# Kernel optimization log

Hardware: AMD Instinct MI355X
Metric: run time of the kernel (lower is better)

The kernel has to match this reference:

```python
import jax, jax.numpy as jnp
import numpy as np

N, E, F, H, RBF = 50000, 400000, 128, 8, 100
HD = F // H
CUTOFF = 6.0

def _xavier(k, shape):
    fan_out, fan_in = shape
    lim = (6.0 / (fan_in + fan_out)) ** 0.5
    return jax.random.uniform(k, shape, minval=-lim, maxval=lim, dtype=jnp.float32)

def setup_inputs():
    key = jax.random.key(0)
    ks = jax.random.split(key, 16)
    x = jax.random.normal(ks[0], (N, F), jnp.float32)
    vec = jax.random.normal(ks[1], (N, 3, F), jnp.float32)
    edge_index = jax.random.randint(ks[2], (2, E), 0, N, dtype=jnp.int32)
    r_ij = jax.random.uniform(ks[3], (E,), jnp.float32) * CUTOFF
    d_ij = jax.random.normal(ks[4], (E, 3), jnp.float32)
    d_ij = d_ij / jnp.linalg.norm(d_ij, axis=-1, keepdims=True)
    f_ij = jax.random.normal(ks[5], (E, RBF), jnp.float32)
    return dict(
        x=x, vec=vec, edge_index=edge_index, r_ij=r_ij, f_ij=f_ij, d_ij=d_ij,
        ln_w=jnp.ones((F,), jnp.float32), ln_b=jnp.zeros((F,), jnp.float32),
        Wq=_xavier(ks[6], (F, F)), bq=jnp.zeros((F,), jnp.float32),
        Wk=_xavier(ks[7], (F, F)), bk=jnp.zeros((F,), jnp.float32),
        Wv=_xavier(ks[8], (3 * F, F)), bv=jnp.zeros((3 * F,), jnp.float32),
        Wvec=_xavier(ks[9], (3 * F, F)), bvec=jnp.zeros((3 * F,), jnp.float32),
        Wo=_xavier(ks[10], (3 * F, F)), bo=jnp.zeros((3 * F,), jnp.float32),
        Wdk=_xavier(ks[11], (F, RBF)), bdk=jnp.zeros((F,), jnp.float32),
        Wdv=_xavier(ks[12], (3 * F, RBF)), bdv=jnp.zeros((3 * F,), jnp.float32),
    )

def _cutoff(r):
    # CosineCutoff with cutoff_lower=0
    return 0.5 * (jnp.cos(r * (jnp.pi / CUTOFF)) + 1.0) * (r < CUTOFF).astype(r.dtype)

def reference(x, vec, edge_index, r_ij, f_ij, d_ij, ln_w, ln_b, Wq, bq, Wk, bk,
              Wv, bv, Wvec, bvec, Wo, bo, Wdk, bdk, Wdv, bdv):
    src, dst = edge_index[0], edge_index[1]  # PyG: x_j = x[src], x_i = x[dst], aggregate at dst
    mu = x.mean(-1, keepdims=True)
    var = ((x - mu) ** 2).mean(-1, keepdims=True)
    xn = (x - mu) / jnp.sqrt(var + 1e-5) * ln_w + ln_b
    q = (xn @ Wq.T + bq).reshape(N, H, HD)
    k = (xn @ Wk.T + bk).reshape(N, H, HD)
    v = (xn @ Wv.T + bv).reshape(N, H, 3 * HD)
    vp = vec @ Wvec.T + bvec  # (N,3,3F)
    vec1, vec2, vec3 = vp[..., :F], vp[..., F:2 * F], vp[..., 2 * F:]
    vec_dot = (vec1 * vec2).sum(axis=1)  # (N,F)
    vec_h = vec.reshape(N, 3, H, HD)
    dk = jax.nn.silu(f_ij @ Wdk.T + bdk).reshape(E, H, HD)
    dv = jax.nn.silu(f_ij @ Wdv.T + bdv).reshape(E, H, 3 * HD)
    # edge-wise messages
    attn = jax.nn.silu((q[dst] * k[src] * dk).sum(-1)) * _cutoff(r_ij)[:, None]  # (E,H)
    v_j = v[src] * dv
    xm, v1m, v2m = v_j[..., :HD], v_j[..., HD:2 * HD], v_j[..., 2 * HD:]
    xm = xm * attn[..., None]  # (E,H,HD)
    vecm = vec_h[src] * v1m[:, None] + v2m[:, None] * d_ij[:, :, None, None]  # (E,3,H,HD)
    # scatter-add to destination nodes
    x_agg = jax.ops.segment_sum(xm.reshape(E, F), dst, num_segments=N)
    vec_agg = jax.ops.segment_sum(vecm.reshape(E, 3 * F), dst, num_segments=N).reshape(N, 3, F)
    o = x_agg @ Wo.T + bo
    o1, o2, o3 = o[:, :F], o[:, F:2 * F], o[:, 2 * F:]
    dx = vec_dot * o2 + o3
    dvec = vec3 * o1[:, None, :] + vec_agg
    return dx, dvec
```

## Files before the change

### kernel.cpp

```cpp
#include <hip/hip_runtime.h>

#define N_NODES 50000
#define N_EDGES 400000

typedef __bf16 bf16x8 __attribute__((ext_vector_type(8)));
typedef float f32x4 __attribute__((ext_vector_type(4)));

__device__ __forceinline__ float bflo(uint u){ union{uint i; float f;} v; v.i = u<<16; return v.f; }
__device__ __forceinline__ float bfhi(uint u){ union{uint i; float f;} v; v.i = u & 0xffff0000u; return v.f; }
__device__ __forceinline__ float bf2f(ushort u){ union{uint i; float f;} v; v.i = ((uint)u)<<16; return v.f; }
__device__ __forceinline__ ushort f2bf(float f){
  union{float f; uint i;} v; v.f = f;
  uint r = (v.i + 0x7fffu + ((v.i>>16)&1u))>>16;
  return (ushort)r;
}
__device__ __forceinline__ uint pack2(float a, float b){
  return (uint)f2bf(a) | ((uint)f2bf(b)<<16);
}

__global__ __launch_bounds__(256) void f32_to_bf16(
    const float* __restrict__ in, ushort* __restrict__ out, int n)
{
  int i = blockIdx.x*256 + threadIdx.x;
  if (i < n) out[i] = f2bf(in[i]);
}

__global__ __launch_bounds__(256) void convert_pad(
    const float* __restrict__ in, ushort* __restrict__ out,
    int rows, int Kin, int Kout)
{
  int i = blockIdx.x*256 + threadIdx.x;
  if (i >= rows*Kout) return;
  int r = i / Kout, c = i - r*Kout;
  out[i] = (c < Kin) ? f2bf(in[(size_t)r*Kin + c]) : (ushort)0;
}

__global__ __launch_bounds__(256) void ln_kernel(
    const float* __restrict__ x, const float* __restrict__ w,
    const float* __restrict__ b, ushort* __restrict__ xn)
{
  int n = blockIdx.x*4 + (threadIdx.x>>6);
  if (n >= N_NODES) return;
  int lane = threadIdx.x & 63;
  float2 xp = ((const float2*)x)[(size_t)n*64 + lane];
  float x0 = xp.x, x1 = xp.y;
  float s = x0 + x1, s2 = x0*x0 + x1*x1;
  #pragma unroll
  for (int off=1; off<64; off<<=1){ s += __shfl_xor(s,off); s2 += __shfl_xor(s2,off); }
  float mu  = s*(1.0f/128.0f);
  float var = s2*(1.0f/128.0f) - mu*mu;
  float inv = 1.0f/sqrtf(var + 1e-5f);
  float2 wp = ((const float2*)w)[lane];
  float2 bp = ((const float2*)b)[lane];
  float y0 = (x0-mu)*inv*wp.x + bp.x;
  float y1 = (x1-mu)*inv*wp.y + bp.y;
  ((uint*)xn)[(size_t)n*64 + lane] = pack2(y0, y1);
}

__global__ __launch_bounds__(256) void hist_kernel(
    const int* __restrict__ ei, int* __restrict__ cnt)
{
  int e = blockIdx.x*256 + threadIdx.x;
  if (e < N_EDGES) atomicAdd(&cnt[ei[N_EDGES + e]], 1);
}

__global__ __launch_bounds__(1024) void scan_kernel(
    const int* __restrict__ cnt, int* __restrict__ offs, int* __restrict__ cursor)
{
  __shared__ int wsum[16];
  __shared__ int carry_s;
  int tid = threadIdx.x, lane = tid & 63, wid = tid >> 6;
  if (tid == 0) carry_s = 0;
  __syncthreads();
  for (int base = 0; base < N_NODES; base += 1024){
    int i = base + tid;
    int v = (i < N_NODES) ? cnt[i] : 0;
    int x = v;
    #pragma unroll
    for (int o=1;o<64;o<<=1){ int t=__shfl_up(x,o); if (lane>=o) x+=t; }
    if (lane == 63) wsum[wid] = x;
    __syncthreads();
    if (wid == 0){
      int ws = (lane < 16) ? wsum[lane] : 0;
      #pragma unroll
      for (int o=1;o<16;o<<=1){ int t=__shfl_up(ws,o); if (lane>=o) ws+=t; }
      if (lane < 16) wsum[lane] = ws;
    }
    __syncthreads();
    int wpre = (wid > 0) ? wsum[wid-1] : 0;
    int exc = x + wpre - v;
    int total = wsum[15];
    int o_ = carry_s + exc;
    if (i < N_NODES){ offs[i] = o_; cursor[i] = o_; }
    __syncthreads();
    if (tid == 0) carry_s += total;
    __syncthreads();
  }
  if (tid == 0) offs[N_NODES] = carry_s;
}

__global__ __launch_bounds__(256) void scatter_kernel(
    const int* __restrict__ ei, const float* __restrict__ rij,
    const float* __restrict__ dij, int* __restrict__ cursor,
    int* __restrict__ perm, int* __restrict__ srcs, int* __restrict__ dsts,
    float4* __restrict__ ed)
{
  int e = blockIdx.x*256 + threadIdx.x;
  if (e >= N_EDGES) return;
  int d = ei[N_EDGES + e];
  int pos = atomicAdd(&cursor[d], 1);
  perm[pos] = e;
  srcs[pos] = ei[e];
  dsts[pos] = d;
  ed[pos] = make_float4(rij[e], dij[3*(size_t)e], dij[3*(size_t)e+1], dij[3*(size_t)e+2]);
}

__global__ __launch_bounds__(256) void gather_fij(
    int st, int len, const int* __restrict__ perm,
    const float* __restrict__ fij, ushort* __restrict__ out)
{
  int p = blockIdx.x*4 + (threadIdx.x>>6);
  if (p >= len) return;
  int lane = threadIdx.x & 63;
  int eo = perm[st + p];
  uint val = 0;
  if (lane < 50){
    float2 f = *(const float2*)(fij + (size_t)eo*100 + 2*lane);
    val = pack2(f.x, f.y);
  }
  ((uint*)out)[(size_t)p*64 + lane] = val;
}

#define LDP 40

template<int MODE, int AF32, int SWZ>
__global__ __launch_bounds__(256) void gemm_bt(
    const void* __restrict__ Av, const ushort* __restrict__ W,
    const ushort* __restrict__ W2,
    const float* __restrict__ bias, const float* __restrict__ bias2,
    void* Cptr, const void* aux1, void* aux2,
    int M, int K, int Nc)
{
  __shared__ ushort As[128*LDP];
  __shared__ ushort Bs[128*LDP];
  __shared__ ushort Bs2[(MODE==7) ? 128*LDP : 2];
  const int tid = threadIdx.x;
  int bx, by;
  if (SWZ){
    int nby = Nc >> 7;
    int nwg = gridDim.x;
    int id  = blockIdx.x;
    int q = nwg >> 3, r = nwg & 7;
    int xcd = id & 7, iq = id >> 3;
    int base = (xcd < r) ? xcd*(q+1) : r*(q+1) + (xcd - r)*q;
    int L = base + iq;
    bx = L / nby; by = L - bx*nby;
  } else { bx = blockIdx.x; by = blockIdx.y; }
  const int row0 = bx*128, col0 = by*128;
  const int wave = tid>>6, lane = tid&63;
  const int wm = (wave>>1)*64, wn = (wave&1)*64;
  const int lr = lane&15, lq = lane>>4;
  f32x4 acc[4][4] = {};
  f32x4 acc2[4][4] = {};

  for (int k0=0; k0<K; k0+=32){
    #pragma unroll
    for (int rnd=0; rnd<2; rnd++){
      int e4 = (rnd*256 + tid)*8;
      int r = e4>>5, c = e4&31;
      int gk = k0 + c;
      {
        int gr = row0 + r;
        if (AF32){
          const float* Af = (const float*)Av;
          uint2 lo, hi;
          if (gr < M && gk + 8 <= K){
            const float* p = Af + (size_t)gr*K + gk;
            float4 f0 = *(const float4*)p;
            float4 f1 = *(const float4*)(p+4);
            lo = make_uint2(pack2(f0.x,f0.y), pack2(f0.z,f0.w));
            hi = make_uint2(pack2(f1.x,f1.y), pack2(f1.z,f1.w));
          } else {
            float t[8];
            #pragma unroll
            for (int i=0;i<8;i++) t[i] = (gr<M && gk+i<K) ? Af[(size_t)gr*K + gk + i] : 0.0f;
            lo = make_uint2(pack2(t[0],t[1]), pack2(t[2],t[3]));
            hi = make_uint2(pack2(t[4],t[5]), pack2(t[6],t[7]));
          }
          *(uint2*)&As[r*LDP + c]     = lo;
          *(uint2*)&As[r*LDP + c + 4] = hi;
        } else {
          const ushort* Ab = (const ushort*)Av;
          if (gr < M && gk + 8 <= K){
            uint4 t = *(const uint4*)(Ab + (size_t)gr*K + gk);
            *(uint4*)&As[r*LDP + c] = t;
          } else {
            ushort t[8];
            #pragma unroll
            for (int i=0;i<8;i++) t[i] = (gr<M && gk+i<K) ? Ab[(size_t)gr*K + gk + i] : (ushort)0;
            *(uint2*)&As[r*LDP + c]     = make_uint2(((uint)t[0])|((uint)t[1]<<16), ((uint)t[2])|((uint)t[3]<<16));
            *(uint2*)&As[r*LDP + c + 4] = make_uint2(((uint)t[4])|((uint)t[5]<<16), ((uint)t[6])|((uint)t[7]<<16));
          }
        }
      }
      {
        int gr = col0 + r;
        if (gr < Nc && gk + 8 <= K){
          uint4 t = *(const uint4*)(W + (size_t)gr*K + gk);
          *(uint4*)&Bs[r*LDP + c] = t;
        } else {
          ushort t[8];
          #pragma unroll
          for (int i=0;i<8;i++) t[i] = (gr<Nc && gk+i<K) ? W[(size_t)gr*K + gk + i] : (ushort)0;
          *(uint2*)&Bs[r*LDP + c]     = make_uint2(((uint)t[0])|((uint)t[1]<<16), ((uint)t[2])|((uint)t[3]<<16));
          *(uint2*)&Bs[r*LDP + c + 4] = make_uint2(((uint)t[4])|((uint)t[5]<<16), ((uint)t[6])|((uint)t[7]<<16));
        }
      }
      if (MODE==7){
        int gr = col0 + r;
        if (gr < Nc && gk + 8 <= K){
          uint4 t = *(const uint4*)(W2 + (size_t)gr*K + gk);
          *(uint4*)&Bs2[r*LDP + c] = t;
        } else {
          ushort t[8];
          #pragma unroll
          for (int i=0;i<8;i++) t[i] = (gr<Nc && gk+i<K) ? W2[(size_t)gr*K + gk + i] : (ushort)0;
          *(uint2*)&Bs2[r*LDP + c]     = make_uint2(((uint)t[0])|((uint)t[1]<<16), ((uint)t[2])|((uint)t[3]<<16));
          *(uint2*)&Bs2[r*LDP + c + 4] = make_uint2(((uint)t[4])|((uint)t[5]<<16), ((uint)t[6])|((uint)t[7]<<16));
        }
      }
    }
    __syncthreads();
    bf16x8 af[4], bfr[4];
    #pragma unroll
    for (int i=0;i<4;i++) af[i]  = *(const bf16x8*)&As[(wm + i*16 + lr)*LDP + lq*8];
    #pragma unroll
    for (int i=0;i<4;i++) bfr[i] = *(const bf16x8*)&Bs[(wn + i*16 + lr)*LDP + lq*8];
    #pragma unroll
    for (int i=0;i<4;i++)
      #pragma unroll
      for (int j=0;j<4;j++)
        acc[i][j] = __builtin_amdgcn_mfma_f32_16x16x32_bf16(af[i], bfr[j], acc[i][j], 0,0,0);
    if (MODE==7){
      bf16x8 bfr2[4];
      #pragma unroll
      for (int i=0;i<4;i++) bfr2[i] = *(const bf16x8*)&Bs2[(wn + i*16 + lr)*LDP + lq*8];
      #pragma unroll
      for (int i=0;i<4;i++)
        #pragma unroll
        for (int j=0;j<4;j++)
          acc2[i][j] = __builtin_amdgcn_mfma_f32_16x16x32_bf16(af[i], bfr2[j], acc2[i][j], 0,0,0);
    }
    __syncthreads();
  }

  const ushort* aux1b = (const ushort*)aux1;
  const float*  aux1f = (const float*)aux1;
  float* aux2f = (float*)aux2;

  #pragma unroll
  for (int i=0;i<4;i++){
    int rowb = row0 + wm + i*16 + lq*4;
    #pragma unroll
    for (int j=0;j<4;j++){
      int c = col0 + wn + j*16 + lr;
      float bv  = bias  ? bias[c]  : 0.0f;
      float bv2 = (MODE==7) ? bias2[c] : 0.0f;
      #pragma unroll
      for (int rg=0; rg<4; rg++){
        int row = rowb + rg;
        if (row < M){
          float vv = acc[i][j][rg] + bv;
          size_t idx = (size_t)row*Nc + c;
          if (MODE==0){
            ((ushort*)Cptr)[idx] = f2bf(vv);
          } else if (MODE==1){
            vv = vv/(1.0f + __expf(-vv));
            ((ushort*)Cptr)[idx] = f2bf(vv);
          } else if (MODE==4){
            aux2f[idx] *= vv;
          } else if (MODE==5){
            float r = aux1f[idx] + vv;
            ((float*)Cptr)[idx] = r;
          } else if (MODE==6){
            float o1 = bf2f(aux1b[(size_t)(row/3)*Nc + c]);
            float r = vv*o1 + aux2f[idx];
            ((float*)Cptr)[idx] = r;
          } else if (MODE==7){
            float vv2 = acc2[i][j][rg] + bv2;
            atomicAdd(aux2f + (size_t)(row/3)*Nc + c, vv*vv2);
          }
        }
      }
    }
  }
}

#define AGG_G 16

__global__ __launch_bounds__(256) void agg_kernel(
    int st, int len,
    const int* __restrict__ dsts, const int* __restrict__ srcs,
    const float4* __restrict__ ed,
    const ushort* __restrict__ qk, const ushort* __restrict__ v,
    const ushort* __restrict__ vecb, const ushort* __restrict__ dkv,
    float* __restrict__ x_agg, float* __restrict__ vec_agg)
{
  int w = blockIdx.x*4 + (threadIdx.x>>6);
  int p0 = st + w*AGG_G;
  int pend = st + len;
  if (p0 >= pend) return;
  int p1 = p0 + AGG_G; if (p1 > pend) p1 = pend;
  int lane = threadIdx.x & 63;

  const uint* qk32  = (const uint*)qk;
  const uint* v32   = (const uint*)v;
  const uint* vec32 = (const uint*)vecb;
  const uint* dkv32 = (const uint*)dkv;
  int h  = lane>>3;
  int cb = h*24 + (lane&7);
  int f0 = 2*lane;

  int dcur = -1;
  uint qp = 0;
  float xa0=0.f, xa1=0.f;
  float vA0=0.f, vA1=0.f, vB0=0.f, vB1=0.f, vC0=0.f, vC1=0.f;

  for (int p=p0; p<p1; ++p){
    int d = dsts[p];
    if (d != dcur){
      if (dcur >= 0){
        float* xrow = x_agg + (size_t)dcur*128;
        atomicAdd(xrow+f0,   xa0);
        atomicAdd(xrow+f0+1, xa1);
        float* vrow = vec_agg + (size_t)dcur*384;
        atomicAdd(vrow+f0,       vA0); atomicAdd(vrow+f0+1,     vA1);
        atomicAdd(vrow+128+f0,   vB0); atomicAdd(vrow+128+f0+1, vB1);
        atomicAdd(vrow+256+f0,   vC0); atomicAdd(vrow+256+f0+1, vC1);
      }
      dcur = d;
      qp = qk32[(size_t)d*128 + lane];
      xa0=xa1=vA0=vA1=vB0=vB1=vC0=vC1=0.f;
    }
    int src = srcs[p];
    float4 e = ed[p];
    uint kp = qk32[(size_t)src*128 + 64 + lane];
    const uint* dr = dkv32 + (size_t)(p-st)*256;
    uint dkp = dr[lane];
    float s = bflo(qp)*bflo(kp)*bflo(dkp) + bfhi(qp)*bfhi(kp)*bfhi(dkp);
    s += __shfl_xor(s,1); s += __shfl_xor(s,2); s += __shfl_xor(s,4);
    float r = e.x;
    float cut = (r < 6.0f) ? 0.5f*(__cosf(r*0.52359877559829887f) + 1.0f) : 0.0f;
    float attn = (s/(1.0f + __expf(-s))) * cut;

    size_t vr = (size_t)src*192;
    const uint* dv = dr + 64;
    uint vx = v32[vr+cb],    dvx = dv[cb];
    uint v1 = v32[vr+cb+8],  dv1 = dv[cb+8];
    uint v2 = v32[vr+cb+16], dv2 = dv[cb+16];
    xa0 += bflo(vx)*bflo(dvx)*attn;
    xa1 += bfhi(vx)*bfhi(dvx)*attn;
    float v1m0 = bflo(v1)*bflo(dv1), v1m1 = bfhi(v1)*bfhi(dv1);
    float v2m0 = bflo(v2)*bflo(dv2), v2m1 = bfhi(v2)*bfhi(dv2);
    uint va  = vec32[vr + lane];
    uint vbx = vec32[vr + 64 + lane];
    uint vc  = vec32[vr + 128 + lane];
    vA0 += bflo(va)*v1m0  + v2m0*e.y;  vA1 += bfhi(va)*v1m1  + v2m1*e.y;
    vB0 += bflo(vbx)*v1m0 + v2m0*e.z;  vB1 += bfhi(vbx)*v1m1 + v2m1*e.z;
    vC0 += bflo(vc)*v1m0  + v2m0*e.w;  vC1 += bfhi(vc)*v1m1  + v2m1*e.w;
  }
  if (dcur >= 0){
    float* xrow = x_agg + (size_t)dcur*128;
    atomicAdd(xrow+f0,   xa0);
    atomicAdd(xrow+f0+1, xa1);
    float* vrow = vec_agg + (size_t)dcur*384;
    atomicAdd(vrow+f0,       vA0); atomicAdd(vrow+f0+1,     vA1);
    atomicAdd(vrow+128+f0,   vB0); atomicAdd(vrow+128+f0+1, vB1);
    atomicAdd(vrow+256+f0,   vC0); atomicAdd(vrow+256+f0+1, vC1);
  }
}

extern "C" void kernel_launch(void* const* d_in, const int* in_sizes, int n_in,
                              void* d_out, int out_size, void* d_ws, size_t ws_size,
                              hipStream_t stream)
{
  (void)in_sizes; (void)n_in; (void)out_size;
  constexpr int Nn = N_NODES, Ee = N_EDGES;
  const float* x    = (const float*)d_in[0];
  const float* vec  = (const float*)d_in[1];
  const int*   eidx = (const int*)  d_in[2];
  const float* rij  = (const float*)d_in[3];
  const float* fij  = (const float*)d_in[4];
  const float* dij  = (const float*)d_in[5];
  const float* lnw  = (const float*)d_in[6];
  const float* lnb  = (const float*)d_in[7];
  const float* Wq   = (const float*)d_in[8];
  const float* bq   = (const float*)d_in[9];
  const float* Wk   = (const float*)d_in[10];
  const float* bk   = (const float*)d_in[11];
  const float* Wv   = (const float*)d_in[12];
  const float* bv   = (const float*)d_in[13];
  const float* Wvec = (const float*)d_in[14];
  const float* bvec = (const float*)d_in[15];
  const float* Wo   = (const float*)d_in[16];
  const float* bo   = (const float*)d_in[17];
  const float* Wdk  = (const float*)d_in[18];
  const float* bdk  = (const float*)d_in[19];
  const float* Wdv  = (const float*)d_in[20];
  const float* bdv  = (const float*)d_in[21];

  float*  outf = (float*)d_out;
  ushort* qkb  = (ushort*)d_out;
  float*  vdot = outf;
  float*  vagg = outf + (size_t)Nn*128;

  char* w = (char*)d_ws;
  size_t off = 0;
  auto alloc = [&](size_t bytes){ size_t o = off; off += (bytes + 255) & ~(size_t)255; return o; };

  ushort* WqkB  = (ushort*)(w + alloc(32768*2));
  ushort* WvB   = (ushort*)(w + alloc(49152*2));
  ushort* WvecB = (ushort*)(w + alloc(49152*2));
  ushort* WoB   = (ushort*)(w + alloc(49152*2));
  ushort* WdkvP = (ushort*)(w + alloc(512*128*2));
  float*  bqk   = (float*) (w + alloc(256*4));
  float*  bdkv  = (float*) (w + alloc(512*4));
  ushort* vecb  = (ushort*)(w + alloc((size_t)3*Nn*128*2));
  ushort* vb    = (ushort*)(w + alloc((size_t)Nn*384*2));
  float*  xagg  = (float*) (w + alloc((size_t)Nn*128*4));
  ushort* o1b   = (ushort*)(w + alloc((size_t)Nn*128*2));
  int*    cnt   = (int*)   (w + alloc((size_t)Nn*4));
  int*    offs  = (int*)   (w + alloc((size_t)(Nn+1)*4));
  int*    cursor= (int*)   (w + alloc((size_t)Nn*4));
  int*    perm  = (int*)   (w + alloc((size_t)Ee*4));
  int*    srcs  = (int*)   (w + alloc((size_t)Ee*4));
  int*    dsts  = (int*)   (w + alloc((size_t)Ee*4));
  float4* ed    = (float4*)(w + alloc((size_t)Ee*16));

  size_t sc_off = off;
  char*  sc = w + sc_off;
  ushort* xn = (ushort*)sc;
  long long chunkC = (ws_size > sc_off) ? (long long)((ws_size - sc_off) / 1280) : 128;
  if (chunkC > 98304) chunkC = 98304;
  chunkC &= ~127LL;
  if (chunkC < 128) chunkC = 128;
  ushort* fijb = (ushort*)sc;
  ushort* dkvc = (ushort*)(sc + (size_t)chunkC*256);

  f32_to_bf16<<<(16384+255)/256, 256, 0, stream>>>(Wq,   WqkB,        16384);
  f32_to_bf16<<<(16384+255)/256, 256, 0, stream>>>(Wk,   WqkB+16384,  16384);
  f32_to_bf16<<<(49152+255)/256, 256, 0, stream>>>(Wv,   WvB,   49152);
  f32_to_bf16<<<(49152+255)/256, 256, 0, stream>>>(Wvec, WvecB, 49152);
  f32_to_bf16<<<(49152+255)/256, 256, 0, stream>>>(Wo,   WoB,   49152);
  convert_pad<<<(128*128+255)/256, 256, 0, stream>>>(Wdk, WdkvP,           128, 100, 128);
  convert_pad<<<(384*128+255)/256, 256, 0, stream>>>(Wdv, WdkvP + 128*128, 384, 100, 128);
  f32_to_bf16<<<(3*Nn*128+255)/256, 256, 0, stream>>>(vec, vecb, 3*Nn*128);
  hipMemcpyAsync(bqk,        bq,  128*4, hipMemcpyDeviceToDevice, stream);
  hipMemcpyAsync(bqk + 128,  bk,  128*4, hipMemcpyDeviceToDevice, stream);
  hipMemcpyAsync(bdkv,       bdk, 128*4, hipMemcpyDeviceToDevice, stream);
  hipMemcpyAsync(bdkv + 128, bdv, 384*4, hipMemcpyDeviceToDevice, stream);

  hipMemsetAsync(xagg, 0, (size_t)Nn*128*4, stream);
  hipMemsetAsync(vagg, 0, (size_t)3*Nn*128*4, stream);
  hipMemsetAsync(cnt,  0, (size_t)Nn*4, stream);

  hist_kernel<<<(Ee+255)/256, 256, 0, stream>>>(eidx, cnt);
  scan_kernel<<<1, 1024, 0, stream>>>(cnt, offs, cursor);
  scatter_kernel<<<(Ee+255)/256, 256, 0, stream>>>(eidx, rij, dij, cursor, perm, srcs, dsts, ed);

  ln_kernel<<<(Nn+3)/4, 256, 0, stream>>>(x, lnw, lnb, xn);

  gemm_bt<0,0,0><<<dim3((Nn+127)/128, 2), 256, 0, stream>>>(xn, WqkB, nullptr, bqk, nullptr, qkb, nullptr, nullptr, Nn, 128, 256);
  gemm_bt<0,0,0><<<dim3((Nn+127)/128, 3), 256, 0, stream>>>(xn, WvB,  nullptr, bv,  nullptr, vb,  nullptr, nullptr, Nn, 128, 384);

  for (int st = 0; st < Ee; st += (int)chunkC){
    int len = Ee - st; if (len > (int)chunkC) len = (int)chunkC;
    gather_fij<<<(len+3)/4, 256, 0, stream>>>(st, len, perm, fij, fijb);
    int nbx = (len+127)/128;
    gemm_bt<1,0,1><<<dim3(nbx*4, 1), 256, 0, stream>>>(fijb, WdkvP, nullptr, bdkv, nullptr, dkvc, nullptr, nullptr, len, 128, 512);
    int waves = (len + AGG_G - 1)/AGG_G;
    agg_kernel<<<(waves+3)/4, 256, 0, stream>>>(st, len, dsts, srcs, ed, qkb, vb, vecb, dkvc, xagg, vagg);
  }

  hipMemsetAsync(vdot, 0, (size_t)Nn*128*4, stream);
  gemm_bt<7,0,0><<<dim3((3*Nn+127)/128, 1), 256, 0, stream>>>(vecb, WvecB, WvecB + 128*128, bvec, bvec + 128, nullptr, nullptr, vdot, 3*Nn, 128, 128);

  gemm_bt<0,1,0><<<dim3((Nn+127)/128, 1), 256, 0, stream>>>(xagg, WoB,            nullptr, bo,       nullptr, o1b,    nullptr, nullptr, Nn, 128, 128);
  gemm_bt<4,1,0><<<dim3((Nn+127)/128, 1), 256, 0, stream>>>(xagg, WoB + 128*128,  nullptr, bo + 128, nullptr, nullptr, nullptr, vdot,   Nn, 128, 128);
  gemm_bt<5,1,0><<<dim3((Nn+127)/128, 1), 256, 0, stream>>>(xagg, WoB + 256*128,  nullptr, bo + 256, nullptr, outf,   vdot,    nullptr, Nn, 128, 128);
  gemm_bt<6,0,0><<<dim3((3*Nn+127)/128, 1), 256, 0, stream>>>(vecb, WvecB + 256*128, nullptr, bvec + 256, nullptr, outf + (size_t)Nn*128, o1b, vagg, 3*Nn, 128, 128);
}
```

Baseline: 1.616 ms.

## Fuse fij gather into dkv GEMM, merge output GEMMs, prefetch edges in aggregation

The f_ij row gather and bf16 packing now run inside a dedicated dkv GEMM that stages all four K-slices in shared memory, so the separate gather kernel and its scratch buffer go away. The three Wo projection GEMMs are merged into one kernel that computes o1/o2/o3 together and applies the vec_dot epilogue. vec_dot is now written as per-component products instead of atomic adds plus a memset, and is summed in the final epilogue. The aggregation loop software-prefetches the next edge's operands to hide gather latency, at the cost of more registers and larger shared memory in the new kernels.

```diff
diff --git a/kernel.cpp b/kernel.cpp
--- a/kernel.cpp
+++ b/kernel.cpp
@@ -115,27 +115,88 @@
   ed[pos] = make_float4(rij[e], dij[3*(size_t)e], dij[3*(size_t)e+1], dij[3*(size_t)e+2]);
 }
 
-__global__ __launch_bounds__(256) void gather_fij(
+#define LDP 40
+
+__global__ __launch_bounds__(256) void dkv_gemm(
     int st, int len, const int* __restrict__ perm,
-    const float* __restrict__ fij, ushort* __restrict__ out)
-{
-  int p = blockIdx.x*4 + (threadIdx.x>>6);
-  if (p >= len) return;
-  int lane = threadIdx.x & 63;
-  int eo = perm[st + p];
-  uint val = 0;
-  if (lane < 50){
-    float2 f = *(const float2*)(fij + (size_t)eo*100 + 2*lane);
-    val = pack2(f.x, f.y);
-  }
-  ((uint*)out)[(size_t)p*64 + lane] = val;
-}
-
-#define LDP 40
-
-template<int MODE, int AF32, int SWZ>
+    const float* __restrict__ fij, const ushort* __restrict__ W,
+    const float* __restrict__ bias, ushort* __restrict__ out)
+{
+  __shared__ int rowid[128];
+  __shared__ ushort As4[4][128*LDP];
+  __shared__ ushort Bs[128*LDP];
+  const int tid = threadIdx.x;
+  int nwg = gridDim.x;
+  int id  = blockIdx.x;
+  int q = nwg >> 3, r8 = nwg & 7;
+  int xcd = id & 7, iq = id >> 3;
+  int base = (xcd < r8) ? xcd*(q+1) : r8*(q+1) + (xcd - r8)*q;
+  int L = base + iq;
+  const int bx = L >> 2, by = L & 3;
+  const int row0 = bx*128, col0 = by*128;
+  const int wave = tid>>6, lane = tid&63;
+  const int wm = (wave>>1)*64, wn = (wave&1)*64;
+  const int lr = lane&15, lq = lane>>4;
+  f32x4 acc[4][4] = {};
+
+  if (tid < 128) rowid[tid] = (row0 + tid < len) ? perm[st + row0 + tid] : -1;
+  __syncthreads();
+  #pragma unroll
+  for (int it=0; it<32; ++it){
+    int idx = it*256 + tid;
+    int rr = idx>>6, c = idx&63;
+    int eo = rowid[rr];
+    uint val = 0u;
+    if (eo >= 0 && c < 50){
+      float2 f = *(const float2*)(fij + (size_t)eo*100 + 2*c);
+      val = pack2(f.x, f.y);
+    }
+    *(uint*)&As4[c>>4][rr*LDP + 2*(c&15)] = val;
+  }
+  for (int k0=0; k0<4; ++k0){
+    #pragma unroll
+    for (int rnd=0; rnd<2; rnd++){
+      int e4 = (rnd*256 + tid)*8;
+      int rr = e4>>5, c = e4&31;
+      uint4 t = *(const uint4*)(W + (size_t)(col0+rr)*128 + k0*32 + c);
+      *(uint4*)&Bs[rr*LDP + c] = t;
+    }
+    __syncthreads();
+    bf16x8 af[4], bfr[4];
+    #pragma unroll
+    for (int i=0;i<4;i++) af[i]  = *(const bf16x8*)&As4[k0][(wm + i*16 + lr)*LDP + lq*8];
+    #pragma unroll
+    for (int i=0;i<4;i++) bfr[i] = *(const bf16x8*)&Bs[(wn + i*16 + lr)*LDP + lq*8];
+    #pragma unroll
+    for (int i=0;i<4;i++)
+      #pragma unroll
+      for (int j=0;j<4;j++)
+        acc[i][j] = __builtin_amdgcn_mfma_f32_16x16x32_bf16(af[i], bfr[j], acc[i][j], 0,0,0);
+    __syncthreads();
+  }
+  #pragma unroll
+  for (int i=0;i<4;i++){
+    int rowb = wm + i*16 + lq*4;
+    #pragma unroll
+    for (int j=0;j<4;j++){
+      int c = col0 + wn + j*16 + lr;
+      float bv = bias[c];
+      #pragma unroll
+      for (int rg=0; rg<4; rg++){
+        int row = row0 + rowb + rg;
+        if (row < len){
+          float vv = acc[i][j][rg] + bv;
+          vv = vv/(1.0f + __expf(-vv));
+          out[(size_t)row*512 + c] = f2bf(vv);
+        }
+      }
+    }
+  }
+}
+
+template<int MODE>
 __global__ __launch_bounds__(256) void gemm_bt(
-    const void* __restrict__ Av, const ushort* __restrict__ W,
+    const ushort* __restrict__ A, const ushort* __restrict__ W,
     const ushort* __restrict__ W2,
     const float* __restrict__ bias, const float* __restrict__ bias2,
     void* Cptr, const void* aux1, void* aux2,
@@ -143,20 +204,9 @@
 {
   __shared__ ushort As[128*LDP];
   __shared__ ushort Bs[128*LDP];
-  __shared__ ushort Bs2[(MODE==7) ? 128*LDP : 2];
+  __shared__ ushort Bs2[(MODE==8) ? 128*LDP : 2];
   const int tid = threadIdx.x;
-  int bx, by;
-  if (SWZ){
-    int nby = Nc >> 7;
-    int nwg = gridDim.x;
-    int id  = blockIdx.x;
-    int q = nwg >> 3, r = nwg & 7;
-    int xcd = id & 7, iq = id >> 3;
-    int base = (xcd < r) ? xcd*(q+1) : r*(q+1) + (xcd - r)*q;
-    int L = base + iq;
-    bx = L / nby; by = L - bx*nby;
-  } else { bx = blockIdx.x; by = blockIdx.y; }
-  const int row0 = bx*128, col0 = by*128;
+  const int row0 = blockIdx.x*128, col0 = blockIdx.y*128;
   const int wave = tid>>6, lane = tid&63;
   const int wm = (wave>>1)*64, wn = (wave&1)*64;
   const int lr = lane&15, lq = lane>>4;
@@ -171,62 +221,29 @@
       int gk = k0 + c;
       {
         int gr = row0 + r;
-        if (AF32){
-          const float* Af = (const float*)Av;
-          uint2 lo, hi;
-          if (gr < M && gk + 8 <= K){
-            const float* p = Af + (size_t)gr*K + gk;
-            float4 f0 = *(const float4*)p;
-            float4 f1 = *(const float4*)(p+4);
-            lo = make_uint2(pack2(f0.x,f0.y), pack2(f0.z,f0.w));
-            hi = make_uint2(pack2(f1.x,f1.y), pack2(f1.z,f1.w));
-          } else {
-            float t[8];
-            #pragma unroll
-            for (int i=0;i<8;i++) t[i] = (gr<M && gk+i<K) ? Af[(size_t)gr*K + gk + i] : 0.0f;
-            lo = make_uint2(pack2(t[0],t[1]), pack2(t[2],t[3]));
-            hi = make_uint2(pack2(t[4],t[5]), pack2(t[6],t[7]));
-          }
-          *(uint2*)&As[r*LDP + c]     = lo;
-          *(uint2*)&As[r*LDP + c + 4] = hi;
+        if (gr < M){
+          uint4 t = *(const uint4*)(A + (size_t)gr*K + gk);
+          *(uint4*)&As[r*LDP + c] = t;
         } else {
-          const ushort* Ab = (const ushort*)Av;
-          if (gr < M && gk + 8 <= K){
-            uint4 t = *(const uint4*)(Ab + (size_t)gr*K + gk);
-            *(uint4*)&As[r*LDP + c] = t;
-          } else {
-            ushort t[8];
-            #pragma unroll
-            for (int i=0;i<8;i++) t[i] = (gr<M && gk+i<K) ? Ab[(size_t)gr*K + gk + i] : (ushort)0;
-            *(uint2*)&As[r*LDP + c]     = make_uint2(((uint)t[0])|((uint)t[1]<<16), ((uint)t[2])|((uint)t[3]<<16));
-            *(uint2*)&As[r*LDP + c + 4] = make_uint2(((uint)t[4])|((uint)t[5]<<16), ((uint)t[6])|((uint)t[7]<<16));
-          }
+          *(uint4*)&As[r*LDP + c] = make_uint4(0,0,0,0);
         }
       }
       {
         int gr = col0 + r;
-        if (gr < Nc && gk + 8 <= K){
+        if (gr < Nc){
           uint4 t = *(const uint4*)(W + (size_t)gr*K + gk);
           *(uint4*)&Bs[r*LDP + c] = t;
         } else {
-          ushort t[8];
-          #pragma unroll
-          for (int i=0;i<8;i++) t[i] = (gr<Nc && gk+i<K) ? W[(size_t)gr*K + gk + i] : (ushort)0;
-          *(uint2*)&Bs[r*LDP + c]     = make_uint2(((uint)t[0])|((uint)t[1]<<16), ((uint)t[2])|((uint)t[3]<<16));
-          *(uint2*)&Bs[r*LDP + c + 4] = make_uint2(((uint)t[4])|((uint)t[5]<<16), ((uint)t[6])|((uint)t[7]<<16));
+          *(uint4*)&Bs[r*LDP + c] = make_uint4(0,0,0,0);
         }
       }
-      if (MODE==7){
+      if (MODE==8){
         int gr = col0 + r;
-        if (gr < Nc && gk + 8 <= K){
+        if (gr < Nc){
           uint4 t = *(const uint4*)(W2 + (size_t)gr*K + gk);
           *(uint4*)&Bs2[r*LDP + c] = t;
         } else {
-          ushort t[8];
-          #pragma unroll
-          for (int i=0;i<8;i++) t[i] = (gr<Nc && gk+i<K) ? W2[(size_t)gr*K + gk + i] : (ushort)0;
-          *(uint2*)&Bs2[r*LDP + c]     = make_uint2(((uint)t[0])|((uint)t[1]<<16), ((uint)t[2])|((uint)t[3]<<16));
-          *(uint2*)&Bs2[r*LDP + c + 4] = make_uint2(((uint)t[4])|((uint)t[5]<<16), ((uint)t[6])|((uint)t[7]<<16));
+          *(uint4*)&Bs2[r*LDP + c] = make_uint4(0,0,0,0);
         }
       }
     }
@@ -241,7 +258,7 @@
       #pragma unroll
       for (int j=0;j<4;j++)
         acc[i][j] = __builtin_amdgcn_mfma_f32_16x16x32_bf16(af[i], bfr[j], acc[i][j], 0,0,0);
-    if (MODE==7){
+    if (MODE==8){
       bf16x8 bfr2[4];
       #pragma unroll
       for (int i=0;i<4;i++) bfr2[i] = *(const bf16x8*)&Bs2[(wn + i*16 + lr)*LDP + lq*8];
@@ -255,7 +272,6 @@
   }
 
   const ushort* aux1b = (const ushort*)aux1;
-  const float*  aux1f = (const float*)aux1;
   float* aux2f = (float*)aux2;
 
   #pragma unroll
@@ -265,7 +281,7 @@
     for (int j=0;j<4;j++){
       int c = col0 + wn + j*16 + lr;
       float bv  = bias  ? bias[c]  : 0.0f;
-      float bv2 = (MODE==7) ? bias2[c] : 0.0f;
+      float bv2 = (MODE==8) ? bias2[c] : 0.0f;
       #pragma unroll
       for (int rg=0; rg<4; rg++){
         int row = rowb + rg;
@@ -274,21 +290,12 @@
           size_t idx = (size_t)row*Nc + c;
           if (MODE==0){
             ((ushort*)Cptr)[idx] = f2bf(vv);
-          } else if (MODE==1){
-            vv = vv/(1.0f + __expf(-vv));
-            ((ushort*)Cptr)[idx] = f2bf(vv);
-          } else if (MODE==4){
-            aux2f[idx] *= vv;
-          } else if (MODE==5){
-            float r = aux1f[idx] + vv;
-            ((float*)Cptr)[idx] = r;
           } else if (MODE==6){
             float o1 = bf2f(aux1b[(size_t)(row/3)*Nc + c]);
-            float r = vv*o1 + aux2f[idx];
-            ((float*)Cptr)[idx] = r;
-          } else if (MODE==7){
+            ((float*)Cptr)[idx] = vv*o1 + aux2f[idx];
+          } else if (MODE==8){
             float vv2 = acc2[i][j][rg] + bv2;
-            atomicAdd(aux2f + (size_t)(row/3)*Nc + c, vv*vv2);
+            ((float*)Cptr)[idx] = vv*vv2;
           }
         }
       }
@@ -296,7 +303,97 @@
   }
 }
 
+__global__ __launch_bounds__(256) void final_gemm(
+    const float* __restrict__ A, const ushort* __restrict__ W,
+    const float* __restrict__ bias, const float* __restrict__ prod,
+    float* __restrict__ dx, ushort* __restrict__ o1b)
+{
+  __shared__ ushort As[128*LDP];
+  __shared__ ushort Bs[384*LDP];
+  const int tid = threadIdx.x;
+  const int row0 = blockIdx.x*128;
+  const int wave = tid>>6, lane = tid&63;
+  const int wm = (wave>>1)*64, wn = (wave&1)*64;
+  const int lr = lane&15, lq = lane>>4;
+  f32x4 acc[3][4][4] = {};
+
+  for (int k0=0; k0<128; k0+=32){
+    #pragma unroll
+    for (int rnd=0; rnd<2; rnd++){
+      int e4 = (rnd*256 + tid)*8;
+      int r = e4>>5, c = e4&31;
+      int gr = row0 + r;
+      uint2 lo, hi;
+      if (gr < N_NODES){
+        const float* p = A + (size_t)gr*128 + k0 + c;
+        float4 f0 = *(const float4*)p;
+        float4 f1 = *(const float4*)(p+4);
+        lo = make_uint2(pack2(f0.x,f0.y), pack2(f0.z,f0.w));
+        hi = make_uint2(pack2(f1.x,f1.y), pack2(f1.z,f1.w));
+      } else { lo = make_uint2(0,0); hi = make_uint2(0,0); }
+      *(uint2*)&As[r*LDP + c]     = lo;
+      *(uint2*)&As[r*LDP + c + 4] = hi;
+    }
+    #pragma unroll
+    for (int rnd=0; rnd<6; rnd++){
+      int e4 = (rnd*256 + tid)*8;
+      int r = e4>>5, c = e4&31;
+      uint4 t = *(const uint4*)(W + (size_t)r*128 + k0 + c);
+      *(uint4*)&Bs[r*LDP + c] = t;
+    }
+    __syncthreads();
+    bf16x8 af[4];
+    #pragma unroll
+    for (int i=0;i<4;i++) af[i] = *(const bf16x8*)&As[(wm + i*16 + lr)*LDP + lq*8];
+    #pragma unroll
+    for (int g=0; g<3; g++){
+      bf16x8 bfr[4];
+      #pragma unroll
+      for (int i=0;i<4;i++) bfr[i] = *(const bf16x8*)&Bs[(g*128 + wn + i*16 + lr)*LDP + lq*8];
+      #pragma unroll
+      for (int i=0;i<4;i++)
+        #pragma unroll
+        for (int j=0;j<4;j++)
+          acc[g][i][j] = __builtin_amdgcn_mfma_f32_16x16x32_bf16(af[i], bfr[j], acc[g][i][j], 0,0,0);
+    }
+    __syncthreads();
+  }
+
+  #pragma unroll
+  for (int i=0;i<4;i++){
+    int rowb = row0 + wm + i*16 + lq*4;
+    #pragma unroll
+    for (int j=0;j<4;j++){
+      int c = wn + j*16 + lr;
+      float b1 = bias[c], b2 = bias[128+c], b3 = bias[256+c];
+      #pragma unroll
+      for (int rg=0; rg<4; rg++){
+        int row = rowb + rg;
+        if (row < N_NODES){
+          float o1 = acc[0][i][j][rg] + b1;
+          float o2 = acc[1][i][j][rg] + b2;
+          float o3 = acc[2][i][j][rg] + b3;
+          size_t pb = (size_t)row*384 + c;
+          float vd = prod[pb] + prod[pb+128] + prod[pb+256];
+          dx[(size_t)row*128 + c] = vd*o2 + o3;
+          o1b[(size_t)row*128 + c] = f2bf(o1);
+        }
+      }
+    }
+  }
+}
+
 #define AGG_G 16
+
+#define AGG_FLUSH() do{ \
+    float* xrow = x_agg + (size_t)dcur*128; \
+    atomicAdd(xrow+f0,   xa0); \
+    atomicAdd(xrow+f0+1, xa1); \
+    float* vrow = vec_agg + (size_t)dcur*384; \
+    atomicAdd(vrow+f0,       vA0); atomicAdd(vrow+f0+1,     vA1); \
+    atomicAdd(vrow+128+f0,   vB0); atomicAdd(vrow+128+f0+1, vB1); \
+    atomicAdd(vrow+256+f0,   vC0); atomicAdd(vrow+256+f0+1, vC1); \
+  }while(0)
 
 __global__ __launch_bounds__(256) void agg_kernel(
     int st, int len,
@@ -326,58 +423,60 @@
   float xa0=0.f, xa1=0.f;
   float vA0=0.f, vA1=0.f, vB0=0.f, vB1=0.f, vC0=0.f, vC1=0.f;
 
+  int src = srcs[p0], d = dsts[p0];
+  float4 e = ed[p0];
+  const uint* dr = dkv32 + (size_t)(p0-st)*256;
+  uint kp  = qk32[(size_t)src*128 + 64 + lane];
+  uint qpc = qk32[(size_t)d*128 + lane];
+  uint dkp = dr[lane];
+  uint dvx = dr[64+cb], dv1 = dr[64+cb+8], dv2 = dr[64+cb+16];
+  size_t vr = (size_t)src*192;
+  uint vx = v32[vr+cb], v1 = v32[vr+cb+8], v2 = v32[vr+cb+16];
+  uint va = vec32[vr+lane], vbx = vec32[vr+64+lane], vc = vec32[vr+128+lane];
+
   for (int p=p0; p<p1; ++p){
-    int d = dsts[p];
+    bool hasn = (p+1 < p1);
+    int srcn=0, dn=0; float4 en=make_float4(0,0,0,0);
+    uint kpn=0, qpcn=0, dkpn=0, dvxn=0, dv1n=0, dv2n=0;
+    uint vxn=0, v1n=0, v2n=0, van=0, vbxn=0, vcn=0;
+    if (hasn){
+      srcn = srcs[p+1]; dn = dsts[p+1]; en = ed[p+1];
+      const uint* drn = dkv32 + (size_t)(p+1-st)*256;
+      kpn  = qk32[(size_t)srcn*128 + 64 + lane];
+      qpcn = (dn != d) ? qk32[(size_t)dn*128 + lane] : qpc;
+      dkpn = drn[lane];
+      dvxn = drn[64+cb]; dv1n = drn[64+cb+8]; dv2n = drn[64+cb+16];
+      size_t vrn = (size_t)srcn*192;
+      vxn = v32[vrn+cb]; v1n = v32[vrn+cb+8]; v2n = v32[vrn+cb+16];
+      van = vec32[vrn+lane]; vbxn = vec32[vrn+64+lane]; vcn = vec32[vrn+128+lane];
+    }
     if (d != dcur){
-      if (dcur >= 0){
-        float* xrow = x_agg + (size_t)dcur*128;
-        atomicAdd(xrow+f0,   xa0);
-        atomicAdd(xrow+f0+1, xa1);
-        float* vrow = vec_agg + (size_t)dcur*384;
-        atomicAdd(vrow+f0,       vA0); atomicAdd(vrow+f0+1,     vA1);
-        atomicAdd(vrow+128+f0,   vB0); atomicAdd(vrow+128+f0+1, vB1);
-        atomicAdd(vrow+256+f0,   vC0); atomicAdd(vrow+256+f0+1, vC1);
-      }
+      if (dcur >= 0) AGG_FLUSH();
       dcur = d;
-      qp = qk32[(size_t)d*128 + lane];
+      qp = qpc;
       xa0=xa1=vA0=vA1=vB0=vB1=vC0=vC1=0.f;
     }
-    int src = srcs[p];
-    float4 e = ed[p];
-    uint kp = qk32[(size_t)src*128 + 64 + lane];
-    const uint* dr = dkv32 + (size_t)(p-st)*256;
-    uint dkp = dr[lane];
     float s = bflo(qp)*bflo(kp)*bflo(dkp) + bfhi(qp)*bfhi(kp)*bfhi(dkp);
     s += __shfl_xor(s,1); s += __shfl_xor(s,2); s += __shfl_xor(s,4);
     float r = e.x;
     float cut = (r < 6.0f) ? 0.5f*(__cosf(r*0.52359877559829887f) + 1.0f) : 0.0f;
     float attn = (s/(1.0f + __expf(-s))) * cut;
 
-    size_t vr = (size_t)src*192;
-    const uint* dv = dr + 64;
-    uint vx = v32[vr+cb],    dvx = dv[cb];
-    uint v1 = v32[vr+cb+8],  dv1 = dv[cb+8];
-    uint v2 = v32[vr+cb+16], dv2 = dv[cb+16];
     xa0 += bflo(vx)*bflo(dvx)*attn;
     xa1 += bfhi(vx)*bfhi(dvx)*attn;
     float v1m0 = bflo(v1)*bflo(dv1), v1m1 = bfhi(v1)*bfhi(dv1);
     float v2m0 = bflo(v2)*bflo(dv2), v2m1 = bfhi(v2)*bfhi(dv2);
-    uint va  = vec32[vr + lane];
-    uint vbx = vec32[vr + 64 + lane];
-    uint vc  = vec32[vr + 128 + lane];
     vA0 += bflo(va)*v1m0  + v2m0*e.y;  vA1 += bfhi(va)*v1m1  + v2m1*e.y;
     vB0 += bflo(vbx)*v1m0 + v2m0*e.z;  vB1 += bfhi(vbx)*v1m1 + v2m1*e.z;
     vC0 += bflo(vc)*v1m0  + v2m0*e.w;  vC1 += bfhi(vc)*v1m1  + v2m1*e.w;
-  }
-  if (dcur >= 0){
-    float* xrow = x_agg + (size_t)dcur*128;
-    atomicAdd(xrow+f0,   xa0);
-    atomicAdd(xrow+f0+1, xa1);
-    float* vrow = vec_agg + (size_t)dcur*384;
-    atomicAdd(vrow+f0,       vA0); atomicAdd(vrow+f0+1,     vA1);
-    atomicAdd(vrow+128+f0,   vB0); atomicAdd(vrow+128+f0+1, vB1);
-    atomicAdd(vrow+256+f0,   vC0); atomicAdd(vrow+256+f0+1, vC1);
-  }
+
+    if (hasn){
+      src=srcn; d=dn; e=en; kp=kpn; qpc=qpcn; dkp=dkpn;
+      dvx=dvxn; dv1=dv1n; dv2=dv2n; vx=vxn; v1=v1n; v2=v2n;
+      va=van; vbx=vbxn; vc=vcn;
+    }
+  }
+  if (dcur >= 0) AGG_FLUSH();
 }
 
 extern "C" void kernel_launch(void* const* d_in, const int* in_sizes, int n_in,
@@ -411,7 +510,6 @@
 
   float*  outf = (float*)d_out;
   ushort* qkb  = (ushort*)d_out;
-  float*  vdot = outf;
   float*  vagg = outf + (size_t)Nn*128;
 
   char* w = (char*)d_ws;
@@ -440,12 +538,12 @@
   size_t sc_off = off;
   char*  sc = w + sc_off;
   ushort* xn = (ushort*)sc;
-  long long chunkC = (ws_size > sc_off) ? (long long)((ws_size - sc_off) / 1280) : 128;
+  long long chunkC = (ws_size > sc_off) ? (long long)((ws_size - sc_off) / 1024) : 128;
   if (chunkC > 98304) chunkC = 98304;
   chunkC &= ~127LL;
   if (chunkC < 128) chunkC = 128;
-  ushort* fijb = (ushort*)sc;
-  ushort* dkvc = (ushort*)(sc + (size_t)chunkC*256);
+  ushort* dkvc = (ushort*)sc;
+  float*  prod = (float*)sc;
 
   f32_to_bf16<<<(16384+255)/256, 256, 0, stream>>>(Wq,   WqkB,        16384);
   f32_to_bf16<<<(16384+255)/256, 256, 0, stream>>>(Wk,   WqkB+16384,  16384);
@@ -470,23 +568,20 @@
 
   ln_kernel<<<(Nn+3)/4, 256, 0, stream>>>(x, lnw, lnb, xn);
 
-  gemm_bt<0,0,0><<<dim3((Nn+127)/128, 2), 256, 0, stream>>>(xn, WqkB, nullptr, bqk, nullptr, qkb, nullptr, nullptr, Nn, 128, 256);
-  gemm_bt<0,0,0><<<dim3((Nn+127)/128, 3), 256, 0, stream>>>(xn, WvB,  nullptr, bv,  nullptr, vb,  nullptr, nullptr, Nn, 128, 384);
+  gemm_bt<0><<<dim3((Nn+127)/128, 2), 256, 0, stream>>>(xn, WqkB, nullptr, bqk, nullptr, qkb, nullptr, nullptr, Nn, 128, 256);
+  gemm_bt<0><<<dim3((Nn+127)/128, 3), 256, 0, stream>>>(xn, WvB,  nullptr, bv,  nullptr, vb,  nullptr, nullptr, Nn, 128, 384);
 
   for (int st = 0; st < Ee; st += (int)chunkC){
     int len = Ee - st; if (len > (int)chunkC) len = (int)chunkC;
-    gather_fij<<<(len+3)/4, 256, 0, stream>>>(st, len, perm, fij, fijb);
     int nbx = (len+127)/128;
-    gemm_bt<1,0,1><<<dim3(nbx*4, 1), 256, 0, stream>>>(fijb, WdkvP, nullptr, bdkv, nullptr, dkvc, nullptr, nullptr, len, 128, 512);
+    dkv_gemm<<<nbx*4, 256, 0, stream>>>(st, len, perm, fij, WdkvP, bdkv, dkvc);
     int waves = (len + AGG_G - 1)/AGG_G;
     agg_kernel<<<(waves+3)/4, 256, 0, stream>>>(st, len, dsts, srcs, ed, qkb, vb, vecb, dkvc, xagg, vagg);
   }
 
-  hipMemsetAsync(vdot, 0, (size_t)Nn*128*4, stream);
-  gemm_bt<7,0,0><<<dim3((3*Nn+127)/128, 1), 256, 0, stream>>>(vecb, WvecB, WvecB + 128*128, bvec, bvec + 128, nullptr, nullptr, vdot, 3*Nn, 128, 128);
-
-  gemm_bt<0,1,0><<<dim3((Nn+127)/128, 1), 256, 0, stream>>>(xagg, WoB,            nullptr, bo,       nullptr, o1b,    nullptr, nullptr, Nn, 128, 128);
-  gemm_bt<4,1,0><<<dim3((Nn+127)/128, 1), 256, 0, stream>>>(xagg, WoB + 128*128,  nullptr, bo + 128, nullptr, nullptr, nullptr, vdot,   Nn, 128, 128);
-  gemm_bt<5,1,0><<<dim3((Nn+127)/128, 1), 256, 0, stream>>>(xagg, WoB + 256*128,  nullptr, bo + 256, nullptr, outf,   vdot,    nullptr, Nn, 128, 128);
-  gemm_bt<6,0,0><<<dim3((3*Nn+127)/128, 1), 256, 0, stream>>>(vecb, WvecB + 256*128, nullptr, bvec + 256, nullptr, outf + (size_t)Nn*128, o1b, vagg, 3*Nn, 128, 128);
-}
+  gemm_bt<8><<<dim3((3*Nn+127)/128, 1), 256, 0, stream>>>(vecb, WvecB, WvecB + 128*128, bvec, bvec + 128, prod, nullptr, nullptr, 3*Nn, 128, 128);
+
+  final_gemm<<<(Nn+127)/128, 256, 0, stream>>>(xagg, WoB, bo, prod, outf, o1b);
+
+  gemm_bt<6><<<dim3((3*Nn+127)/128, 1), 256, 0, stream>>>(vecb, WvecB + 256*128, nullptr, bvec + 256, nullptr, outf + (size_t)Nn*128, o1b, vagg, 3*Nn, 128, 128);
+}
```

Measured after the change: 1.650 ms. 1.02x slower.
